# Optimization experiments

Measured on AMD Instinct MI355X. Metric: run time of the kernel, lower is better.

The kernel has to match this reference:

```python
import jax, jax.numpy as jnp
import numpy as np

B, T, M, D = 4, 512, 16, 128
P, H = 128, 4
E = P // H


def _glorot(k, shape, fan_in, fan_out):
    lim = np.sqrt(6.0 / (fan_in + fan_out)).astype(np.float32)
    return jax.random.uniform(k, shape, jnp.float32, -lim, lim)


def setup_inputs() -> dict:
    key = jax.random.key(0)
    ks = jax.random.split(key, 12)
    inp = jax.random.normal(ks[0], (B, T, M, D), jnp.float32)
    pos = jax.random.normal(ks[1], (B, T, 1, D), jnp.float32)
    # padding mask: valid time steps per batch element (ensures no fully-masked softmax row)
    lengths = jax.random.randint(ks[2], (B,), T // 2, T + 1)
    mask = jnp.broadcast_to(jnp.arange(T)[None, :, None] < lengths[:, None, None], (B, T, M))
    Wq = _glorot(ks[3], (M, P, D), D, P)
    Wk = _glorot(ks[4], (M, P, D), D, P)
    Wv = _glorot(ks[5], (M, P, D), D, P)
    Wq_t = _glorot(ks[6], (M, P, D), D, P)
    Wk_t = _glorot(ks[7], (M, P, D), D, P)
    Bq = jnp.zeros((M, P), jnp.float32)
    Bk = jnp.zeros((M, P), jnp.float32)
    Bv = jnp.zeros((M, P), jnp.float32)
    Bq_t = jnp.zeros((M, P), jnp.float32)
    Bk_t = jnp.zeros((M, P), jnp.float32)
    return {"inp": inp, "pos": pos, "mask": mask,
            "Wq": Wq, "Bq": Bq, "Wk": Wk, "Bk": Bk, "Wv": Wv, "Bv": Bv,
            "Wq_t": Wq_t, "Bq_t": Bq_t, "Wk_t": Wk_t, "Bk_t": Bk_t}


def reference(inp, pos, mask, Wq, Bq, Wk, Bk, Wv, Bv, Wq_t, Bq_t, Wk_t, Bk_t):
    b, t, m, d = inp.shape
    p = Wq.shape[1]
    h, e = H, P // H
    # per-modality projections: (m,p,d) x (b,t,m,d) -> (b,t,m,p)
    q = jnp.einsum('mpd,btmd->btmp', Wq, inp) + Bq
    k = jnp.einsum('mpd,btmd->btmp', Wk, inp) + Bk
    v = jnp.einsum('mpd,btmd->btmp', Wv, inp) + Bv
    pos0 = pos[:, :, 0, :]  # (b,t,d); broadcasts across m
    q_t = jnp.einsum('mpd,btd->btmp', Wq_t, pos0) + Bq_t
    k_t = jnp.einsum('mpd,btd->btmp', Wk_t, pos0) + Bk_t

    def split_heads(x):  # (b,t,m,p) -> (b,m,h,t,e)
        return x.reshape(b, t, m, h, e).transpose(0, 2, 3, 1, 4)

    q, k, v, q_t, k_t = map(split_heads, (q, k, v, q_t, k_t))
    # dual bilinear score: content + positional
    score = (jnp.einsum('bmhte,bmhse->bmhts', q, k)
             + jnp.einsum('bmhte,bmhse->bmhts', q_t, k_t)) / (2.0 * np.sqrt(e).astype(np.float32))
    causal = jnp.tril(jnp.ones((t, t), bool))  # (t,t)
    score = jnp.where(causal, score, -jnp.inf)
    km = mask.transpose(0, 2, 1)[:, :, None, None, :]  # (b,m,1,1,t)
    score = jnp.where(km, score, -jnp.inf)
    w = jax.nn.softmax(score, axis=-1)
    w = jnp.where(km, w, 0.0)
    w = jnp.where(causal, w, 0.0)
    # dropout is identity at inference (drop_rate ignored)
    out = jnp.einsum('bmhts,bmhse->bmhte', w, v)
    return out.transpose(0, 3, 1, 2, 4).reshape(b, t, m, p)
```

## Files before the change

### kernel.cpp

```cpp
#include <hip/hip_runtime.h>

#define Bn 4
#define Tn 512
#define Mn 16
#define Dn 128
#define Pn 128
#define Hn 4
#define SCALE 0.08838834764831845f

typedef unsigned short u16;
typedef unsigned int u32;
typedef short s16;
typedef __attribute__((ext_vector_type(8))) s16 bf16x8;
typedef __attribute__((ext_vector_type(4))) float f32x4;

__device__ __forceinline__ u16 f2b(float f) {
  u32 x; __builtin_memcpy(&x, &f, 4);
  x += 0x7fffu + ((x >> 16) & 1u);
  return (u16)(x >> 16);
}
__device__ __forceinline__ u32 pack2(float a, float b) {
  return (u32)f2b(a) | ((u32)f2b(b) << 16);
}
__device__ __forceinline__ bf16x8 ld8(const u16* p) {
  bf16x8 r; __builtin_memcpy(&r, p, 16); return r;
}
__device__ __forceinline__ f32x4 mfma16(bf16x8 a, bf16x8 b, f32x4 c) {
  return __builtin_amdgcn_mfma_f32_16x16x32_bf16(a, b, c, 0, 0, 0);
}

__global__ void lengths_kernel(const void* __restrict__ mask, int* __restrict__ len_out) {
  const int b = blockIdx.x;
  __shared__ int cnt[256];
  const u32 w0 = ((const u32*)mask)[0];
  const int mode = (w0 == 1u) ? 0 : (w0 == 0x3F800000u) ? 1
                 : (w0 == 0x3F803F80u) ? 2 : 3;
  int c = 0;
  for (int t = threadIdx.x; t < Tn; t += 256) {
    const size_t idx = ((size_t)b * Tn + t) * Mn;
    int nz;
    if (mode == 0)      nz = (((const int*)mask)[idx] != 0);
    else if (mode == 1) nz = (((const u32*)mask)[idx] != 0u);
    else if (mode == 2) nz = (((const u16*)mask)[idx] != 0);
    else                nz = (((const unsigned char*)mask)[idx] != 0);
    c += nz;
  }
  cnt[threadIdx.x] = c;
  __syncthreads();
  for (int s = 128; s > 0; s >>= 1) {
    if (threadIdx.x < (unsigned)s) cnt[threadIdx.x] += cnt[threadIdx.x + s];
    __syncthreads();
  }
  if (threadIdx.x == 0) len_out[b] = cnt[0];
}

__global__ __launch_bounds__(256) void proj_mfma(
    const float* __restrict__ inp, const float* __restrict__ pos,
    const float* __restrict__ Wq, const float* __restrict__ Bq,
    const float* __restrict__ Wk, const float* __restrict__ Bk,
    const float* __restrict__ Wv, const float* __restrict__ Bv,
    const float* __restrict__ Wqt, const float* __restrict__ Bqt,
    const float* __restrict__ Wkt, const float* __restrict__ Bkt,
    u16* __restrict__ Qa, u16* __restrict__ Ka, u16* __restrict__ Qb,
    u16* __restrict__ Kb, u16* __restrict__ Vt) {
  const int tid = threadIdx.x;
  const int bid = blockIdx.x;
  const int tsel = bid % 5;
  const int m = (bid / 5) % Mn;
  const int rt0 = (bid / (5 * Mn)) * 128;

  const float* W; const float* Bb; int usepos, doscale;
  u16* dst;
  switch (tsel) {
    case 0:  W = Wq;  Bb = Bq;  usepos = 0; doscale = 1; dst = Qa; break;
    case 1:  W = Wk;  Bb = Bk;  usepos = 0; doscale = 0; dst = Ka; break;
    case 2:  W = Wv;  Bb = Bv;  usepos = 0; doscale = 0; dst = Vt; break;
    case 3:  W = Wqt; Bb = Bqt; usepos = 1; doscale = 1; dst = Qb; break;
    default: W = Wkt; Bb = Bkt; usepos = 1; doscale = 0; dst = Kb; break;
  }
  const float* A = usepos ? pos : inp;

  __shared__ __align__(16) u16 Xs[128 * 72];
  __shared__ __align__(16) u16 Ws2[128 * 72];

  const int wv = tid >> 6, lane = tid & 63;
  const int quad = lane >> 4, l16 = lane & 15;

  f32x4 acc[2][8];
#pragma unroll
  for (int qs = 0; qs < 2; ++qs)
#pragma unroll
    for (int n = 0; n < 8; ++n) acc[qs][n] = (f32x4){0.f, 0.f, 0.f, 0.f};

  for (int kh = 0; kh < 2; ++kh) {
    for (int idx = tid; idx < 128 * 16; idx += 256) {
      const int row = idx >> 4, c4 = (idx & 15) * 4, col = kh * 64 + c4;
      const size_t sx = usepos ? ((size_t)(rt0 + row) * Dn + col)
                               : (((size_t)(rt0 + row) * Mn + m) * Dn + col);
      const float4 x = *(const float4*)(A + sx);
      ushort4 xh; xh.x = f2b(x.x); xh.y = f2b(x.y); xh.z = f2b(x.z); xh.w = f2b(x.w);
      *(ushort4*)&Xs[row * 72 + c4] = xh;
      const float4 w = *(const float4*)(W + ((size_t)m * Pn + row) * Dn + col);
      ushort4 wh; wh.x = f2b(w.x); wh.y = f2b(w.y); wh.z = f2b(w.z); wh.w = f2b(w.w);
      *(ushort4*)&Ws2[row * 72 + c4] = wh;
    }
    __syncthreads();
#pragma unroll
    for (int kc = 0; kc < 2; ++kc) {
      const int ko = kc * 32 + quad * 8;
      const bf16x8 a0 = ld8(&Xs[(wv * 32 + l16) * 72 + ko]);
      const bf16x8 a1 = ld8(&Xs[(wv * 32 + 16 + l16) * 72 + ko]);
#pragma unroll
      for (int n = 0; n < 8; ++n) {
        const bf16x8 bn = ld8(&Ws2[(n * 16 + l16) * 72 + ko]);
        acc[0][n] = mfma16(a0, bn, acc[0][n]);
        acc[1][n] = mfma16(a1, bn, acc[1][n]);
      }
    }
    __syncthreads();
  }

  const int b = rt0 >> 9;
  const int tl0 = (rt0 & (Tn - 1)) + wv * 32;
#pragma unroll
  for (int n = 0; n < 8; ++n) {
    const int h = n >> 1, e = (n & 1) * 16 + l16;
    const float bias = Bb[m * Pn + n * 16 + l16];
    const int bmh = (b * Mn + m) * Hn + h;
    if (tsel != 2) {
#pragma unroll
      for (int qs = 0; qs < 2; ++qs)
#pragma unroll
        for (int reg = 0; reg < 4; ++reg) {
          const int t = tl0 + qs * 16 + quad * 4 + reg;
          float v = acc[qs][n][reg] + bias;
          if (doscale) v *= SCALE;
          dst[((size_t)bmh * Tn + t) * 32 + e] = f2b(v);
        }
    } else {
      const size_t rowv = ((size_t)bmh * 32 + e) * Tn;
#pragma unroll
      for (int qs = 0; qs < 2; ++qs) {
        const int t0 = tl0 + qs * 16 + quad * 4;
        uint2 d;
        d.x = pack2(acc[qs][n][0] + bias, acc[qs][n][1] + bias);
        d.y = pack2(acc[qs][n][2] + bias, acc[qs][n][3] + bias);
        *(uint2*)&dst[rowv + t0] = d;
      }
    }
  }
}

__global__ __launch_bounds__(128, 4) void attn_flash(
    const u16* __restrict__ Qa, const u16* __restrict__ Ka,
    const u16* __restrict__ Qb, const u16* __restrict__ Kb,
    const u16* __restrict__ Vt, const int* __restrict__ lens,
    float* __restrict__ out) {
  __shared__ __align__(16) u16 Ps[2 * 32 * 72];

  const int tid = threadIdx.x;
  const int wv = tid >> 6, lane = tid & 63;
  const int quad = lane >> 4, l16 = lane & 15;

  const int wu = blockIdx.x * 2 + wv;
  const int pair = wu & 7;
  const int bmh = wu >> 3;
  const int b = bmh >> 6;
  const int len = lens[b];

  const size_t rowbase = (size_t)bmh * Tn;
  const size_t vbase = (size_t)bmh * 32 * Tn;
  u16* myPs = &Ps[wv * 32 * 72];
  const int mm = (bmh >> 2) & (Mn - 1);
  const int h = bmh & (Hn - 1);

#pragma unroll 1
  for (int half = 0; half < 2; ++half) {
    const int qt = half ? (15 - pair) : pair;
    const int q0 = qt * 32;

    bf16x8 qf[2][2];
#pragma unroll
    for (int qs = 0; qs < 2; ++qs) {
      const size_t r = (rowbase + q0 + qs * 16 + l16) * 32 + quad * 8;
      qf[qs][0] = ld8(Qa + r);
      qf[qs][1] = ld8(Qb + r);
    }

    f32x4 O[2][2];
#pragma unroll
    for (int qs = 0; qs < 2; ++qs)
#pragma unroll
      for (int es = 0; es < 2; ++es) O[qs][es] = (f32x4){0.f, 0.f, 0.f, 0.f};
    float mrow[2] = {-1e30f, -1e30f}, lsum[2] = {0.f, 0.f};

    const int s_hi = min(q0 + 32, len);
    for (int s0 = 0; s0 < s_hi; s0 += 64) {
      f32x4 S[2][4];
#pragma unroll
      for (int st = 0; st < 4; ++st) {
        const size_t kr = (rowbase + s0 + st * 16 + l16) * 32 + quad * 8;
        const bf16x8 k0 = ld8(Ka + kr);
        const bf16x8 k1 = ld8(Kb + kr);
#pragma unroll
        for (int qs = 0; qs < 2; ++qs)
          S[qs][st] = mfma16(k1, qf[qs][1],
                             mfma16(k0, qf[qs][0], (f32x4){0.f, 0.f, 0.f, 0.f}));
      }

#pragma unroll
      for (int qs = 0; qs < 2; ++qs) {
        const int q = q0 + qs * 16 + l16;
        const int qcap = min(q, len - 1);
        const int sb = s0 + quad * 4;
        float cmax = -1e30f;
#pragma unroll
        for (int st = 0; st < 4; ++st)
#pragma unroll
          for (int reg = 0; reg < 4; ++reg) {
            const int s = sb + st * 16 + reg;
            const float v = (s <= qcap) ? S[qs][st][reg] : -1e30f;
            S[qs][st][reg] = v;
            cmax = fmaxf(cmax, v);
          }
        cmax = fmaxf(cmax, __shfl_xor(cmax, 16));
        cmax = fmaxf(cmax, __shfl_xor(cmax, 32));
        const float mnew = fmaxf(mrow[qs], cmax);
        const float alpha = __expf(mrow[qs] - mnew);
        mrow[qs] = mnew;
        float rsum = 0.f;
        u32 pk[4][2];
#pragma unroll
        for (int st = 0; st < 4; ++st) {
          const float p0 = __expf(S[qs][st][0] - mnew);
          const float p1 = __expf(S[qs][st][1] - mnew);
          const float p2 = __expf(S[qs][st][2] - mnew);
          const float p3 = __expf(S[qs][st][3] - mnew);
          rsum += (p0 + p1) + (p2 + p3);
          pk[st][0] = pack2(p0, p1);
          pk[st][1] = pack2(p2, p3);
        }
        rsum += __shfl_xor(rsum, 16);
        rsum += __shfl_xor(rsum, 32);
        lsum[qs] = lsum[qs] * alpha + rsum;
#pragma unroll
        for (int es = 0; es < 2; ++es)
#pragma unroll
          for (int reg = 0; reg < 4; ++reg) O[qs][es][reg] *= alpha;
#pragma unroll
        for (int st = 0; st < 4; ++st) {
          uint2 d; d.x = pk[st][0]; d.y = pk[st][1];
          *(uint2*)&myPs[(qs * 16 + l16) * 72 + st * 16 + quad * 4] = d;
        }
      }

#pragma unroll
      for (int kc = 0; kc < 2; ++kc) {
        const int ko = kc * 32 + quad * 8;
        const bf16x8 pf0 = ld8(&myPs[l16 * 72 + ko]);
        const bf16x8 pf1 = ld8(&myPs[(16 + l16) * 72 + ko]);
        const bf16x8 vf0 = ld8(Vt + vbase + (size_t)l16 * Tn + s0 + ko);
        const bf16x8 vf1 = ld8(Vt + vbase + (size_t)(16 + l16) * Tn + s0 + ko);
        O[0][0] = mfma16(vf0, pf0, O[0][0]);
        O[0][1] = mfma16(vf1, pf0, O[0][1]);
        O[1][0] = mfma16(vf0, pf1, O[1][0]);
        O[1][1] = mfma16(vf1, pf1, O[1][1]);
      }
    }

#pragma unroll
    for (int qs = 0; qs < 2; ++qs) {
      const float linv = 1.0f / lsum[qs];
      const int t = q0 + qs * 16 + l16;
      const size_t ob = (((size_t)b * Tn + t) * Mn + mm) * Pn + h * 32 + quad * 4;
#pragma unroll
      for (int es = 0; es < 2; ++es) {
        float4 o;
        o.x = O[qs][es][0] * linv; o.y = O[qs][es][1] * linv;
        o.z = O[qs][es][2] * linv; o.w = O[qs][es][3] * linv;
        *(float4*)&out[ob + es * 16] = o;
      }
    }
  }
}

extern "C" void kernel_launch(void* const* d_in, const int* in_sizes, int n_in,
                              void* d_out, int out_size, void* d_ws, size_t ws_size,
                              hipStream_t stream) {
  const float* inp = (const float*)d_in[0];
  const float* pos = (const float*)d_in[1];
  const void* mask = d_in[2];
  const float* Wq  = (const float*)d_in[3];
  const float* Bq  = (const float*)d_in[4];
  const float* Wk  = (const float*)d_in[5];
  const float* Bk  = (const float*)d_in[6];
  const float* Wv  = (const float*)d_in[7];
  const float* Bv  = (const float*)d_in[8];
  const float* Wqt = (const float*)d_in[9];
  const float* Bqt = (const float*)d_in[10];
  const float* Wkt = (const float*)d_in[11];
  const float* Bkt = (const float*)d_in[12];
  float* out = (float*)d_out;

  const size_t nA = (size_t)Bn * Mn * Hn * Tn * 32;
  u16* Qa = (u16*)d_ws;
  u16* Ka = Qa + nA;
  u16* Qb = Ka + nA;
  u16* Kb = Qb + nA;
  u16* Vt = Kb + nA;
  int* lens = (int*)(Vt + nA);

  lengths_kernel<<<Bn, 256, 0, stream>>>(mask, lens);
  proj_mfma<<<(Bn * Tn / 128) * Mn * 5, 256, 0, stream>>>(
      inp, pos, Wq, Bq, Wk, Bk, Wv, Bv, Wqt, Bqt, Wkt, Bkt, Qa, Ka, Qb, Kb, Vt);
  attn_flash<<<(Bn * Mn * Hn * 8) / 2, 128, 0, stream>>>(
      Qa, Ka, Qb, Kb, Vt, lens, out);
}
```

Baseline: 149.4 us.

## Pre-convert inputs and weights to bf16 in a prep kernel and transpose projection epilogue

A new prep kernel, merged with the mask-length count, converts inp, pos and all five weight tensors to bf16 once. The projection kernel then loads bf16 directly with 16-byte loads held in registers, and drops one barrier per K-step. For non-V outputs it swaps the MFMA operands so the epilogue writes packed 8-byte stores instead of scattered 2-byte stores. The aim is to cut the repeated fp32 reads and conversions of inp across the five projections and to improve store coalescing, at the cost of an extra full pass over the inputs and more workspace.

```diff
diff --git a/kernel.cpp b/kernel.cpp
--- a/kernel.cpp
+++ b/kernel.cpp
@@ -14,6 +14,8 @@
 typedef __attribute__((ext_vector_type(8))) s16 bf16x8;
 typedef __attribute__((ext_vector_type(4))) float f32x4;
 
+#define NWE (Mn * Pn * Dn)
+
 __device__ __forceinline__ u16 f2b(float f) {
   u32 x; __builtin_memcpy(&x, &f, 4);
   x += 0x7fffu + ((x >> 16) & 1u);
@@ -29,38 +31,72 @@
   return __builtin_amdgcn_mfma_f32_16x16x32_bf16(a, b, c, 0, 0, 0);
 }
 
-__global__ void lengths_kernel(const void* __restrict__ mask, int* __restrict__ len_out) {
-  const int b = blockIdx.x;
-  __shared__ int cnt[256];
-  const u32 w0 = ((const u32*)mask)[0];
-  const int mode = (w0 == 1u) ? 0 : (w0 == 0x3F800000u) ? 1
-                 : (w0 == 0x3F803F80u) ? 2 : 3;
-  int c = 0;
-  for (int t = threadIdx.x; t < Tn; t += 256) {
-    const size_t idx = ((size_t)b * Tn + t) * Mn;
-    int nz;
-    if (mode == 0)      nz = (((const int*)mask)[idx] != 0);
-    else if (mode == 1) nz = (((const u32*)mask)[idx] != 0u);
-    else if (mode == 2) nz = (((const u16*)mask)[idx] != 0);
-    else                nz = (((const unsigned char*)mask)[idx] != 0);
-    c += nz;
-  }
-  cnt[threadIdx.x] = c;
-  __syncthreads();
-  for (int s = 128; s > 0; s >>= 1) {
-    if (threadIdx.x < (unsigned)s) cnt[threadIdx.x] += cnt[threadIdx.x + s];
+__global__ __launch_bounds__(256) void prep(
+    const void* __restrict__ mask, const float* __restrict__ inp,
+    const float* __restrict__ pos, const float* __restrict__ Wq,
+    const float* __restrict__ Wk, const float* __restrict__ Wv,
+    const float* __restrict__ Wqt, const float* __restrict__ Wkt,
+    int* __restrict__ lens, u16* __restrict__ Xb, u16* __restrict__ Pb,
+    u16* __restrict__ Wb) {
+  if (blockIdx.x < Bn) {
+    const int b = blockIdx.x;
+    __shared__ int cnt[256];
+    const u32 w0 = ((const u32*)mask)[0];
+    const int mode = (w0 == 1u) ? 0 : (w0 == 0x3F800000u) ? 1
+                   : (w0 == 0x3F803F80u) ? 2 : 3;
+    int c = 0;
+    for (int t = threadIdx.x; t < Tn; t += 256) {
+      const size_t idx = ((size_t)b * Tn + t) * Mn;
+      int nz;
+      if (mode == 0)      nz = (((const int*)mask)[idx] != 0);
+      else if (mode == 1) nz = (((const u32*)mask)[idx] != 0u);
+      else if (mode == 2) nz = (((const u16*)mask)[idx] != 0);
+      else                nz = (((const unsigned char*)mask)[idx] != 0);
+      c += nz;
+    }
+    cnt[threadIdx.x] = c;
     __syncthreads();
-  }
-  if (threadIdx.x == 0) len_out[b] = cnt[0];
+    for (int s = 128; s > 0; s >>= 1) {
+      if (threadIdx.x < (unsigned)s) cnt[threadIdx.x] += cnt[threadIdx.x + s];
+      __syncthreads();
+    }
+    if (threadIdx.x == 0) lens[b] = cnt[0];
+  }
+
+  const int NI8 = Bn * Tn * Mn * Dn / 8;
+  const int NP8 = Bn * Tn * Dn / 8;
+  const int NW8 = NWE / 8;
+  const int total = NI8 + NP8 + 5 * NW8;
+  for (int u = blockIdx.x * 256 + threadIdx.x; u < total; u += gridDim.x * 256) {
+    const float* s; u16* d; int off;
+    if (u < NI8) { s = inp; d = Xb; off = u; }
+    else if (u < NI8 + NP8) { s = pos; d = Pb; off = u - NI8; }
+    else {
+      const int r = u - NI8 - NP8;
+      const int w = r >> 15; off = r & (NW8 - 1);
+      switch (w) {
+        case 0:  s = Wq;  d = Wb;            break;
+        case 1:  s = Wk;  d = Wb + NWE;      break;
+        case 2:  s = Wv;  d = Wb + 2 * NWE;  break;
+        case 3:  s = Wqt; d = Wb + 3 * NWE;  break;
+        default: s = Wkt; d = Wb + 4 * NWE;  break;
+      }
+    }
+    const float4 a0 = *(const float4*)(s + (size_t)off * 8);
+    const float4 a1 = *(const float4*)(s + (size_t)off * 8 + 4);
+    uint4 dd;
+    dd.x = pack2(a0.x, a0.y); dd.y = pack2(a0.z, a0.w);
+    dd.z = pack2(a1.x, a1.y); dd.w = pack2(a1.z, a1.w);
+    *(uint4*)(d + (size_t)off * 8) = dd;
+  }
 }
 
 __global__ __launch_bounds__(256) void proj_mfma(
-    const float* __restrict__ inp, const float* __restrict__ pos,
-    const float* __restrict__ Wq, const float* __restrict__ Bq,
-    const float* __restrict__ Wk, const float* __restrict__ Bk,
-    const float* __restrict__ Wv, const float* __restrict__ Bv,
-    const float* __restrict__ Wqt, const float* __restrict__ Bqt,
-    const float* __restrict__ Wkt, const float* __restrict__ Bkt,
+    const u16* __restrict__ Xb, const u16* __restrict__ Pb,
+    const u16* __restrict__ Wb,
+    const float* __restrict__ Bq, const float* __restrict__ Bk,
+    const float* __restrict__ Bv, const float* __restrict__ Bqt,
+    const float* __restrict__ Bkt,
     u16* __restrict__ Qa, u16* __restrict__ Ka, u16* __restrict__ Qb,
     u16* __restrict__ Kb, u16* __restrict__ Vt) {
   const int tid = threadIdx.x;
@@ -69,16 +105,16 @@
   const int m = (bid / 5) % Mn;
   const int rt0 = (bid / (5 * Mn)) * 128;
 
-  const float* W; const float* Bb; int usepos, doscale;
-  u16* dst;
+  const float* Bb; int usepos, doscale; u16* dst;
   switch (tsel) {
-    case 0:  W = Wq;  Bb = Bq;  usepos = 0; doscale = 1; dst = Qa; break;
-    case 1:  W = Wk;  Bb = Bk;  usepos = 0; doscale = 0; dst = Ka; break;
-    case 2:  W = Wv;  Bb = Bv;  usepos = 0; doscale = 0; dst = Vt; break;
-    case 3:  W = Wqt; Bb = Bqt; usepos = 1; doscale = 1; dst = Qb; break;
-    default: W = Wkt; Bb = Bkt; usepos = 1; doscale = 0; dst = Kb; break;
-  }
-  const float* A = usepos ? pos : inp;
+    case 0:  Bb = Bq;  usepos = 0; doscale = 1; dst = Qa; break;
+    case 1:  Bb = Bk;  usepos = 0; doscale = 0; dst = Ka; break;
+    case 2:  Bb = Bv;  usepos = 0; doscale = 0; dst = Vt; break;
+    case 3:  Bb = Bqt; usepos = 1; doscale = 1; dst = Qb; break;
+    default: Bb = Bkt; usepos = 1; doscale = 0; dst = Kb; break;
+  }
+  const u16* A = usepos ? Pb : Xb;
+  const u16* Wsrc = Wb + (size_t)tsel * NWE + (size_t)m * Pn * Dn;
 
   __shared__ __align__(16) u16 Xs[128 * 72];
   __shared__ __align__(16) u16 Ws2[128 * 72];
@@ -88,56 +124,68 @@
 
   f32x4 acc[2][8];
 #pragma unroll
-  for (int qs = 0; qs < 2; ++qs)
-#pragma unroll
-    for (int n = 0; n < 8; ++n) acc[qs][n] = (f32x4){0.f, 0.f, 0.f, 0.f};
+  for (int i = 0; i < 2; ++i)
+#pragma unroll
+    for (int n = 0; n < 8; ++n) acc[i][n] = (f32x4){0.f, 0.f, 0.f, 0.f};
+
+  const u16* Als = (tsel == 2) ? Xs : Ws2;
+  const u16* Bls = (tsel == 2) ? Ws2 : Xs;
 
   for (int kh = 0; kh < 2; ++kh) {
-    for (int idx = tid; idx < 128 * 16; idx += 256) {
-      const int row = idx >> 4, c4 = (idx & 15) * 4, col = kh * 64 + c4;
+    bf16x8 xr[4], wr[4];
+#pragma unroll
+    for (int it = 0; it < 4; ++it) {
+      const int c = tid + it * 256;
+      const int row = c >> 3, c8 = (c & 7) * 8, col = kh * 64 + c8;
       const size_t sx = usepos ? ((size_t)(rt0 + row) * Dn + col)
                                : (((size_t)(rt0 + row) * Mn + m) * Dn + col);
-      const float4 x = *(const float4*)(A + sx);
-      ushort4 xh; xh.x = f2b(x.x); xh.y = f2b(x.y); xh.z = f2b(x.z); xh.w = f2b(x.w);
-      *(ushort4*)&Xs[row * 72 + c4] = xh;
-      const float4 w = *(const float4*)(W + ((size_t)m * Pn + row) * Dn + col);
-      ushort4 wh; wh.x = f2b(w.x); wh.y = f2b(w.y); wh.z = f2b(w.z); wh.w = f2b(w.w);
-      *(ushort4*)&Ws2[row * 72 + c4] = wh;
+      xr[it] = ld8(A + sx);
+    }
+#pragma unroll
+    for (int it = 0; it < 4; ++it) {
+      const int c = tid + it * 256;
+      const int row = c >> 3, c8 = (c & 7) * 8, col = kh * 64 + c8;
+      wr[it] = ld8(Wsrc + (size_t)row * Dn + col);
+    }
+    if (kh) __syncthreads();
+#pragma unroll
+    for (int it = 0; it < 4; ++it) {
+      const int c = tid + it * 256;
+      const int row = c >> 3, c8 = (c & 7) * 8;
+      *(bf16x8*)&Xs[row * 72 + c8] = xr[it];
+    }
+#pragma unroll
+    for (int it = 0; it < 4; ++it) {
+      const int c = tid + it * 256;
+      const int row = c >> 3, c8 = (c & 7) * 8;
+      *(bf16x8*)&Ws2[row * 72 + c8] = wr[it];
     }
     __syncthreads();
 #pragma unroll
     for (int kc = 0; kc < 2; ++kc) {
       const int ko = kc * 32 + quad * 8;
-      const bf16x8 a0 = ld8(&Xs[(wv * 32 + l16) * 72 + ko]);
-      const bf16x8 a1 = ld8(&Xs[(wv * 32 + 16 + l16) * 72 + ko]);
+      const bf16x8 a0 = ld8(&Als[(wv * 32 + l16) * 72 + ko]);
+      const bf16x8 a1 = ld8(&Als[(wv * 32 + 16 + l16) * 72 + ko]);
 #pragma unroll
       for (int n = 0; n < 8; ++n) {
-        const bf16x8 bn = ld8(&Ws2[(n * 16 + l16) * 72 + ko]);
+        const bf16x8 bn = ld8(&Bls[(n * 16 + l16) * 72 + ko]);
         acc[0][n] = mfma16(a0, bn, acc[0][n]);
         acc[1][n] = mfma16(a1, bn, acc[1][n]);
       }
     }
-    __syncthreads();
+    if (kh == 0) __syncthreads();
   }
 
   const int b = rt0 >> 9;
-  const int tl0 = (rt0 & (Tn - 1)) + wv * 32;
-#pragma unroll
-  for (int n = 0; n < 8; ++n) {
-    const int h = n >> 1, e = (n & 1) * 16 + l16;
-    const float bias = Bb[m * Pn + n * 16 + l16];
-    const int bmh = (b * Mn + m) * Hn + h;
-    if (tsel != 2) {
-#pragma unroll
-      for (int qs = 0; qs < 2; ++qs)
-#pragma unroll
-        for (int reg = 0; reg < 4; ++reg) {
-          const int t = tl0 + qs * 16 + quad * 4 + reg;
-          float v = acc[qs][n][reg] + bias;
-          if (doscale) v *= SCALE;
-          dst[((size_t)bmh * Tn + t) * 32 + e] = f2b(v);
-        }
-    } else {
+  const int tb = rt0 & (Tn - 1);
+
+  if (tsel == 2) {
+    const int tl0 = tb + wv * 32;
+#pragma unroll
+    for (int n = 0; n < 8; ++n) {
+      const int h = n >> 1, e = (n & 1) * 16 + l16;
+      const float bias = Bb[m * Pn + n * 16 + l16];
+      const int bmh = (b * Mn + m) * Hn + h;
       const size_t rowv = ((size_t)bmh * 32 + e) * Tn;
 #pragma unroll
       for (int qs = 0; qs < 2; ++qs) {
@@ -146,6 +194,24 @@
         d.x = pack2(acc[qs][n][0] + bias, acc[qs][n][1] + bias);
         d.y = pack2(acc[qs][n][2] + bias, acc[qs][n][3] + bias);
         *(uint2*)&dst[rowv + t0] = d;
+      }
+    }
+  } else {
+    const int bmh = (b * Mn + m) * Hn + wv;
+#pragma unroll
+    for (int pf = 0; pf < 2; ++pf) {
+      const int p0 = wv * 32 + pf * 16 + quad * 4;
+      const float4 b4 = *(const float4*)&Bb[m * Pn + p0];
+#pragma unroll
+      for (int tf = 0; tf < 8; ++tf) {
+        const int t = tb + tf * 16 + l16;
+        float v0 = acc[pf][tf][0] + b4.x;
+        float v1 = acc[pf][tf][1] + b4.y;
+        float v2 = acc[pf][tf][2] + b4.z;
+        float v3 = acc[pf][tf][3] + b4.w;
+        if (doscale) { v0 *= SCALE; v1 *= SCALE; v2 *= SCALE; v3 *= SCALE; }
+        uint2 d; d.x = pack2(v0, v1); d.y = pack2(v2, v3);
+        *(uint2*)&dst[((size_t)bmh * Tn + t) * 32 + pf * 16 + quad * 4] = d;
       }
     }
   }
@@ -309,10 +375,14 @@
   u16* Kb = Qb + nA;
   u16* Vt = Kb + nA;
   int* lens = (int*)(Vt + nA);
-
-  lengths_kernel<<<Bn, 256, 0, stream>>>(mask, lens);
+  u16* Xb = (u16*)(lens + 8);
+  u16* Pb = Xb + (size_t)Bn * Tn * Mn * Dn;
+  u16* Wb = Pb + (size_t)Bn * Tn * Dn;
+
+  prep<<<1024, 256, 0, stream>>>(mask, inp, pos, Wq, Wk, Wv, Wqt, Wkt,
+                                 lens, Xb, Pb, Wb);
   proj_mfma<<<(Bn * Tn / 128) * Mn * 5, 256, 0, stream>>>(
-      inp, pos, Wq, Bq, Wk, Bk, Wv, Bv, Wqt, Bqt, Wkt, Bkt, Qa, Ka, Qb, Kb, Vt);
+      Xb, Pb, Wb, Bq, Bk, Bv, Bqt, Bkt, Qa, Ka, Qb, Kb, Vt);
   attn_flash<<<(Bn * Mn * Hn * 8) / 2, 128, 0, stream>>>(
       Qa, Ka, Qb, Kb, Vt, lens, out);
 }
```

Result: no change. 147.7 us (-1.2%).
